# Optimization experiments

Measured on AMD Instinct MI355X. Metric: run time of the kernel, lower is better.

The kernel has to match this reference:

```python
import jax, jax.numpy as jnp
import numpy as np

B, SQ, SK, D, H, F = 8, 512, 1024, 1024, 16, 4096
DK = D // H
NEG_INF = -jnp.inf


def _linear(x, w, b):
    return x @ w + b


def _mha(q, k, v, wq, bq, wk, bk, wv, bv, wo, bo, causal, kv_mask):
    # q: [B,Sq,D], k/v: [B,Sk,D]
    b, sq, d = q.shape
    sk = k.shape[1]
    Q = _linear(q, wq, bq).reshape(b, sq, H, DK).transpose(0, 2, 1, 3)  # [B,H,Sq,dk]
    K = _linear(k, wk, bk).reshape(b, sk, H, DK).transpose(0, 2, 1, 3)
    V = _linear(v, wv, bv).reshape(b, sk, H, DK).transpose(0, 2, 1, 3)
    S = jnp.einsum('bhqd,bhkd->bhqk', Q, K) / jnp.sqrt(jnp.asarray(DK, Q.dtype))
    if kv_mask is not None:
        S = jnp.where(kv_mask[:, None, None, :] == 0, NEG_INF, S)
    if causal:
        tri = jnp.tril(jnp.ones((sq, sk), dtype=bool))
        S = jnp.where(tri, S, NEG_INF)
    A = jax.nn.softmax(S, axis=-1)  # dropout p=0 -> identity
    x = jnp.einsum('bhqk,bhkd->bhqd', A, V).transpose(0, 2, 1, 3).reshape(b, sq, d)
    return _linear(x, wo, bo), A


def _ln(x, g, beta, eps=1e-5):
    mu = jnp.mean(x, axis=-1, keepdims=True)
    var = jnp.mean(jnp.square(x - mu), axis=-1, keepdims=True)
    return (x - mu) * jax.lax.rsqrt(var + eps) * g + beta


def setup_inputs() -> dict:
    key = jax.random.key(0)
    ks = jax.random.split(key, 32)
    s = 0.02
    inp = {
        'x': jax.random.normal(ks[0], (B, SQ, D), jnp.float32),
        'enc_o': jax.random.normal(ks[1], (B, SK, D), jnp.float32),
        'enc_mask': jax.random.randint(ks[2], (B, SK), 0, 2, jnp.int32),
    }
    i = 3
    for pfx in ('a1', 'a2'):
        for nm in ('wq', 'wk', 'wv', 'wo'):
            inp[f'{pfx}_{nm}'] = jax.random.normal(ks[i], (D, D), jnp.float32) * s; i += 1
            inp[f'{pfx}_{nm[1:] and "b" + nm[1:]}'] = jnp.zeros((D,), jnp.float32)
    inp['ff_w1'] = jax.random.normal(ks[i], (D, F), jnp.float32) * s; i += 1
    inp['ff_b1'] = jnp.zeros((F,), jnp.float32)
    inp['ff_w2'] = jax.random.normal(ks[i], (F, D), jnp.float32) * s; i += 1
    inp['ff_b2'] = jnp.zeros((D,), jnp.float32)
    for n in ('ln1', 'ln2', 'ln3'):
        inp[f'{n}_g'] = jnp.ones((D,), jnp.float32)
        inp[f'{n}_b'] = jnp.zeros((D,), jnp.float32)
    return inp


def reference(x, enc_o, enc_mask,
              a1_wq, a1_bq, a1_wk, a1_bk, a1_wv, a1_bv, a1_wo, a1_bo,
              a2_wq, a2_bq, a2_wk, a2_bk, a2_wv, a2_bv, a2_wo, a2_bo,
              ff_w1, ff_b1, ff_w2, ff_b2,
              ln1_g, ln1_b, ln2_g, ln2_b, ln3_g, ln3_b):
    res, _ = _mha(x, x, x, a1_wq, a1_bq, a1_wk, a1_bk, a1_wv, a1_bv, a1_wo, a1_bo,
                  causal=True, kv_mask=None)
    x = _ln(x + res, ln1_g, ln1_b)
    res, attn = _mha(x, enc_o, enc_o, a2_wq, a2_bq, a2_wk, a2_bk, a2_wv, a2_bv, a2_wo, a2_bo,
                     causal=False, kv_mask=enc_mask)
    x = _ln(x + res, ln2_g, ln2_b)
    res = _linear(jax.nn.relu(_linear(x, ff_w1, ff_b1)), ff_w2, ff_b2)
    x = _ln(x + res, ln3_g, ln3_b)
    return (x, attn)
```

## Files before the change

kernel.cpp:

```cpp
#include <hip/hip_runtime.h>
#include <hip/hip_bf16.h>


using bf16 = __hip_bfloat16;
typedef __attribute__((ext_vector_type(8))) short short8;
typedef __attribute__((ext_vector_type(4))) float f32x4;

#define DEVINL __device__ __forceinline__

DEVINL unsigned short bf16bits(float f) {
  __hip_bfloat16 h = __float2bfloat16(f);
  return *reinterpret_cast<unsigned short*>(&h);
}
DEVINL float bits2f(unsigned short u) {
  return __uint_as_float(((unsigned int)u) << 16);
}
DEVINL float tofloat(float f) { return f; }
DEVINL float tofloat(bf16 h) { return __bfloat162float(h); }

#define GLD16(gp, lp) __builtin_amdgcn_global_load_lds( \
    (__attribute__((address_space(1))) const void*)(gp), \
    (__attribute__((address_space(3))) void*)(lp), 16, 0, 0)

struct GemmP {
  const void* A; const bf16* Bt; void* C;
  const float* bias; const int* kmask;
  float scale;
  int M, N, K, lda, ldb, ldc;
  long sAb, sAh, sBb, sBh, sCb, sCh;
};

enum { EPI_BIAS_BF16 = 0, EPI_CAUSAL_BF16, EPI_KMASK_F32, EPI_NONE_BF16,
       EPI_BIAS_F32, EPI_BIAS_RELU_BF16 };

template<int EPI, bool AF32>
__global__ __launch_bounds__(256)
void gemm_k(GemmP p) {
  __shared__ bf16 As[128 * 32];
  __shared__ bf16 Bs[128 * 32];
  const int t = threadIdx.x;
  const int lane = t & 63;
  const int w = t >> 6;
  const int z = blockIdx.z;
  const int zb = z >> 4, zh = z & 15;
  const int m0 = blockIdx.y * 128, n0 = blockIdx.x * 128;

  const bf16* Bb = p.Bt + (long)zb * p.sBb + (long)zh * p.sBh;
  const int fl = lane & 15, fq = lane >> 4;
  const int wm = (w >> 1) * 64, wn = (w & 1) * 64;

  f32x4 acc[4][4];
#pragma unroll
  for (int i = 0; i < 4; ++i)
#pragma unroll
    for (int j = 0; j < 4; ++j) acc[i][j] = (f32x4){0.f, 0.f, 0.f, 0.f};

  const int sr = t >> 2;
  const int sc = (t & 3) * 8;
  char* ldsA = (char*)As + w * 1024;
  char* ldsB = (char*)Bs + w * 1024;

  int brow0 = n0 + sr;      if (brow0 > p.N - 1) brow0 = p.N - 1;
  int brow1 = n0 + sr + 64; if (brow1 > p.N - 1) brow1 = p.N - 1;

  const bf16* Ab16 = nullptr; const float* Af32 = nullptr;
  if (AF32) Af32 = (const float*)p.A + (long)zb * p.sAb + (long)zh * p.sAh;
  else      Ab16 = (const bf16*)p.A + (long)zb * p.sAb + (long)zh * p.sAh;

  for (int k0 = 0; k0 < p.K; k0 += 32) {
    if (!AF32) {
      GLD16(Ab16 + (long)(m0 + sr) * p.lda + k0 + sc, ldsA);
      GLD16(Ab16 + (long)(m0 + sr + 64) * p.lda + k0 + sc, ldsA + 4096);
    } else {
      const int ar = t >> 1, ac = (t & 1) * 16;
      const float* src = Af32 + (long)(m0 + ar) * p.lda + k0 + ac;
      float4 f0 = *(const float4*)(src);
      float4 f1 = *(const float4*)(src + 4);
      float4 f2 = *(const float4*)(src + 8);
      float4 f3 = *(const float4*)(src + 12);
      uint4 q0, q1;
      q0.x = bf16bits(f0.x) | ((unsigned)bf16bits(f0.y) << 16);
      q0.y = bf16bits(f0.z) | ((unsigned)bf16bits(f0.w) << 16);
      q0.z = bf16bits(f1.x) | ((unsigned)bf16bits(f1.y) << 16);
      q0.w = bf16bits(f1.z) | ((unsigned)bf16bits(f1.w) << 16);
      q1.x = bf16bits(f2.x) | ((unsigned)bf16bits(f2.y) << 16);
      q1.y = bf16bits(f2.z) | ((unsigned)bf16bits(f2.w) << 16);
      q1.z = bf16bits(f3.x) | ((unsigned)bf16bits(f3.y) << 16);
      q1.w = bf16bits(f3.z) | ((unsigned)bf16bits(f3.w) << 16);
      *(uint4*)(As + ar * 32 + ac) = q0;
      *(uint4*)(As + ar * 32 + ac + 8) = q1;
    }
    GLD16(Bb + (long)brow0 * p.ldb + k0 + sc, ldsB);
    GLD16(Bb + (long)brow1 * p.ldb + k0 + sc, ldsB + 4096);
    __syncthreads();

    short8 af[4], bfv[4];
#pragma unroll
    for (int i = 0; i < 4; ++i)
      af[i] = *(const short8*)(As + (wm + i * 16 + fl) * 32 + fq * 8);
#pragma unroll
    for (int j = 0; j < 4; ++j)
      bfv[j] = *(const short8*)(Bs + (wn + j * 16 + fl) * 32 + fq * 8);
#pragma unroll
    for (int i = 0; i < 4; ++i)
#pragma unroll
      for (int j = 0; j < 4; ++j)
        acc[i][j] = __builtin_amdgcn_mfma_f32_16x16x32_bf16(af[i], bfv[j], acc[i][j], 0, 0, 0);
    __syncthreads();
  }

  const float NEGINF = -__builtin_inff();
  const long cbase = (long)zb * p.sCb + (long)zh * p.sCh;
#pragma unroll
  for (int i = 0; i < 4; ++i) {
#pragma unroll
    for (int j = 0; j < 4; ++j) {
#pragma unroll
      for (int r = 0; r < 4; ++r) {
        int row = m0 + wm + i * 16 + fq * 4 + r;
        int col = n0 + wn + j * 16 + fl;
        if (col < p.N) {
          float v = acc[i][j][r];
          if (EPI == EPI_BIAS_BF16 || EPI == EPI_BIAS_F32 || EPI == EPI_BIAS_RELU_BF16)
            v += p.bias[col];
          if (EPI == EPI_BIAS_RELU_BF16) v = v > 0.f ? v : 0.f;
          if (EPI == EPI_CAUSAL_BF16) { v *= p.scale; if (col > row) v = NEGINF; }
          if (EPI == EPI_KMASK_F32)   { v *= p.scale; if (p.kmask[zb * 1024 + col] == 0) v = NEGINF; }
          long off = cbase + (long)row * p.ldc + col;
          if (EPI == EPI_KMASK_F32 || EPI == EPI_BIAS_F32) ((float*)p.C)[off] = v;
          else ((bf16*)p.C)[off] = __float2bfloat16(v);
        }
      }
    }
  }
}

__global__ __launch_bounds__(256) void softmax_self_k(bf16* A) {
  const int lane = threadIdx.x & 63;
  const long row = (long)blockIdx.x * 4 + (threadIdx.x >> 6);
  bf16* p = A + row * 512;
  short8 raw = *(const short8*)(p + lane * 8);
  float v[8];
#pragma unroll
  for (int i = 0; i < 8; ++i) v[i] = bits2f((unsigned short)raw[i]);
  float mx = v[0];
#pragma unroll
  for (int i = 1; i < 8; ++i) mx = fmaxf(mx, v[i]);
  for (int off = 32; off; off >>= 1) mx = fmaxf(mx, __shfl_xor(mx, off, 64));
  float s = 0.f;
#pragma unroll
  for (int i = 0; i < 8; ++i) { v[i] = expf(v[i] - mx); s += v[i]; }
  for (int off = 32; off; off >>= 1) s += __shfl_xor(s, off, 64);
  float inv = 1.f / s;
  short8 o;
#pragma unroll
  for (int i = 0; i < 8; ++i) o[i] = (short)bf16bits(v[i] * inv);
  *(short8*)(p + lane * 8) = o;
}

__global__ __launch_bounds__(256) void softmax_cross_k(float* A) {
  const int lane = threadIdx.x & 63;
  const long row = (long)blockIdx.x * 4 + (threadIdx.x >> 6);
  float* p = A + row * 1024;
  float4 v[4];
#pragma unroll
  for (int c = 0; c < 4; ++c) v[c] = *(const float4*)(p + c * 256 + lane * 4);
  float mx = v[0].x;
#pragma unroll
  for (int c = 0; c < 4; ++c) {
    mx = fmaxf(mx, v[c].x); mx = fmaxf(mx, v[c].y);
    mx = fmaxf(mx, v[c].z); mx = fmaxf(mx, v[c].w);
  }
  for (int off = 32; off; off >>= 1) mx = fmaxf(mx, __shfl_xor(mx, off, 64));
  float s = 0.f;
#pragma unroll
  for (int c = 0; c < 4; ++c) {
    v[c].x = expf(v[c].x - mx); s += v[c].x;
    v[c].y = expf(v[c].y - mx); s += v[c].y;
    v[c].z = expf(v[c].z - mx); s += v[c].z;
    v[c].w = expf(v[c].w - mx); s += v[c].w;
  }
  for (int off = 32; off; off >>= 1) s += __shfl_xor(s, off, 64);
  float inv = 1.f / s;
#pragma unroll
  for (int c = 0; c < 4; ++c) {
    v[c].x *= inv; v[c].y *= inv; v[c].z *= inv; v[c].w *= inv;
    *(float4*)(p + c * 256 + lane * 4) = v[c];
  }
}

__global__ __launch_bounds__(256)
void ln_k(const float* __restrict__ x, const float* __restrict__ r,
          const float* __restrict__ g, const float* __restrict__ bt,
          float* __restrict__ outf, bf16* __restrict__ outb) {
  const int lane = threadIdx.x & 63;
  const long row = (long)blockIdx.x * 4 + (threadIdx.x >> 6);
  const float* px = x + row * 1024;
  const float* pr = r + row * 1024;
  float4 v[4];
  float s = 0.f;
#pragma unroll
  for (int c = 0; c < 4; ++c) {
    float4 a = *(const float4*)(px + c * 256 + lane * 4);
    float4 b = *(const float4*)(pr + c * 256 + lane * 4);
    v[c].x = a.x + b.x; v[c].y = a.y + b.y; v[c].z = a.z + b.z; v[c].w = a.w + b.w;
    s += v[c].x + v[c].y + v[c].z + v[c].w;
  }
  for (int off = 32; off; off >>= 1) s += __shfl_xor(s, off, 64);
  float mu = s * (1.f / 1024.f);
  float q = 0.f;
#pragma unroll
  for (int c = 0; c < 4; ++c) {
    float dx = v[c].x - mu, dy = v[c].y - mu, dz = v[c].z - mu, dw = v[c].w - mu;
    q += dx * dx + dy * dy + dz * dz + dw * dw;
  }
  for (int off = 32; off; off >>= 1) q += __shfl_xor(q, off, 64);
  float rs = rsqrtf(q * (1.f / 1024.f) + 1e-5f);
#pragma unroll
  for (int c = 0; c < 4; ++c) {
    int col = c * 256 + lane * 4;
    float4 gg = *(const float4*)(g + col);
    float4 bb = *(const float4*)(bt + col);
    float4 o;
    o.x = (v[c].x - mu) * rs * gg.x + bb.x;
    o.y = (v[c].y - mu) * rs * gg.y + bb.y;
    o.z = (v[c].z - mu) * rs * gg.z + bb.z;
    o.w = (v[c].w - mu) * rs * gg.w + bb.w;
    *(float4*)(outf + row * 1024 + col) = o;
    if (outb) {
      uint2 pk;
      pk.x = bf16bits(o.x) | ((unsigned)bf16bits(o.y) << 16);
      pk.y = bf16bits(o.z) | ((unsigned)bf16bits(o.w) << 16);
      *(uint2*)(outb + row * 1024 + col) = pk;
    }
  }
}

template<typename TI>
__global__ __launch_bounds__(256)
void transpose_k(const TI* __restrict__ in, bf16* __restrict__ out,
                 int R, int C, int ldi, int ldo,
                 long sInb, long sInh, long sOutb, long sOuth) {
  __shared__ float tile[32][33];
  const int zb = blockIdx.z >> 4, zh = blockIdx.z & 15;
  const TI* pin = in + (long)zb * sInb + (long)zh * sInh;
  bf16* pout = out + (long)zb * sOutb + (long)zh * sOuth;
  const int c0 = blockIdx.x * 32, r0 = blockIdx.y * 32;
  const int tx = threadIdx.x & 31, ty = threadIdx.x >> 5;
#pragma unroll
  for (int i = 0; i < 32; i += 8)
    tile[ty + i][tx] = tofloat(pin[(long)(r0 + ty + i) * ldi + c0 + tx]);
  __syncthreads();
#pragma unroll
  for (int i = 0; i < 32; i += 8)
    pout[(long)(c0 + ty + i) * ldo + r0 + tx] = __float2bfloat16(tile[tx][ty + i]);
}

__global__ __launch_bounds__(256) void cvt_k(const float* __restrict__ in,
                                             bf16* __restrict__ out, long n4) {
  long i = (long)blockIdx.x * 256 + threadIdx.x;
  if (i < n4) {
    float4 v = *(const float4*)(in + i * 4);
    uint2 pk;
    pk.x = bf16bits(v.x) | ((unsigned)bf16bits(v.y) << 16);
    pk.y = bf16bits(v.z) | ((unsigned)bf16bits(v.w) << 16);
    *(uint2*)(out + i * 4) = pk;
  }
}

static inline GemmP mkp(const void* A, const bf16* Bt, void* C,
                        const float* bias, const int* km, float sc,
                        int M, int N, int K, int lda, int ldb, int ldc,
                        long sAb, long sAh, long sBb, long sBh, long sCb, long sCh) {
  GemmP p;
  p.A = A; p.Bt = Bt; p.C = C; p.bias = bias; p.kmask = km; p.scale = sc;
  p.M = M; p.N = N; p.K = K; p.lda = lda; p.ldb = ldb; p.ldc = ldc;
  p.sAb = sAb; p.sAh = sAh; p.sBb = sBb; p.sBh = sBh; p.sCb = sCb; p.sCh = sCh;
  return p;
}

extern "C" void kernel_launch(void* const* d_in, const int* in_sizes, int n_in,
                              void* d_out, int out_size, void* d_ws, size_t ws_size,
                              hipStream_t stream) {
  const float* x        = (const float*)d_in[0];
  const float* enc_o    = (const float*)d_in[1];
  const int*   enc_mask = (const int*)d_in[2];
  const float* a1_wq = (const float*)d_in[3];  const float* a1_bq = (const float*)d_in[4];
  const float* a1_wk = (const float*)d_in[5];  const float* a1_bk = (const float*)d_in[6];
  const float* a1_wv = (const float*)d_in[7];  const float* a1_bv = (const float*)d_in[8];
  const float* a1_wo = (const float*)d_in[9];  const float* a1_bo = (const float*)d_in[10];
  const float* a2_wq = (const float*)d_in[11]; const float* a2_bq = (const float*)d_in[12];
  const float* a2_wk = (const float*)d_in[13]; const float* a2_bk = (const float*)d_in[14];
  const float* a2_wv = (const float*)d_in[15]; const float* a2_bv = (const float*)d_in[16];
  const float* a2_wo = (const float*)d_in[17]; const float* a2_bo = (const float*)d_in[18];
  const float* ff_w1 = (const float*)d_in[19]; const float* ff_b1 = (const float*)d_in[20];
  const float* ff_w2 = (const float*)d_in[21]; const float* ff_b2 = (const float*)d_in[22];
  const float* ln1_g = (const float*)d_in[23]; const float* ln1_b = (const float*)d_in[24];
  const float* ln2_g = (const float*)d_in[25]; const float* ln2_b = (const float*)d_in[26];
  const float* ln3_g = (const float*)d_in[27]; const float* ln3_b = (const float*)d_in[28];

  const size_t MB = 1u << 20;
  char* w = (char*)d_ws;
  bf16*  xb   = (bf16*)(w + 0);
  bf16*  encb = (bf16*)(w + 8 * MB);
  float* x1f  = (float*)(w + 24 * MB);
  float* x2f  = (float*)(w + 40 * MB);
  bf16*  xcb  = (bf16*)(w + 56 * MB);
  bf16*  wT   = (bf16*)(w + 64 * MB);
  bf16*  Qb   = (bf16*)(w + 80 * MB);
  bf16*  Kb   = (bf16*)(w + 88 * MB);
  bf16*  Vb   = (bf16*)(w + 104 * MB);
  bf16*  Vt   = (bf16*)(w + 120 * MB);
  bf16*  Ob   = (bf16*)(w + 136 * MB);
  float* res  = (float*)(w + 144 * MB);
  bf16*  Asf  = (bf16*)(w + 160 * MB);

  float* out_x  = (float*)d_out;
  float* attn   = (float*)d_out + 4194304;

  const dim3 blk(256);

  cvt_k<<<4096, blk, 0, stream>>>(x, xb, 1048576);
  cvt_k<<<8192, blk, 0, stream>>>(enc_o, encb, 2097152);

  {
    dim3 tg(32, 32, 1);
    transpose_k<float><<<tg, blk, 0, stream>>>(a1_wq, wT + 0,       1024, 1024, 1024, 1024, 0, 0, 0, 0);
    transpose_k<float><<<tg, blk, 0, stream>>>(a1_wk, wT + 1048576, 1024, 1024, 1024, 1024, 0, 0, 0, 0);
    transpose_k<float><<<tg, blk, 0, stream>>>(a1_wv, wT + 2097152, 1024, 1024, 1024, 1024, 0, 0, 0, 0);
    transpose_k<float><<<tg, blk, 0, stream>>>(a1_wo, wT + 3145728, 1024, 1024, 1024, 1024, 0, 0, 0, 0);
  }
  dim3 gq(8, 32, 1);
  gemm_k<EPI_BIAS_BF16, false><<<gq, blk, 0, stream>>>(
      mkp(xb, wT + 0,       Qb, a1_bq, nullptr, 0.f, 4096, 1024, 1024, 1024, 1024, 1024, 0,0,0,0,0,0));
  gemm_k<EPI_BIAS_BF16, false><<<gq, blk, 0, stream>>>(
      mkp(xb, wT + 1048576, Kb, a1_bk, nullptr, 0.f, 4096, 1024, 1024, 1024, 1024, 1024, 0,0,0,0,0,0));
  gemm_k<EPI_BIAS_BF16, false><<<gq, blk, 0, stream>>>(
      mkp(xb, wT + 2097152, Vb, a1_bv, nullptr, 0.f, 4096, 1024, 1024, 1024, 1024, 1024, 0,0,0,0,0,0));

  gemm_k<EPI_CAUSAL_BF16, false><<<dim3(4, 4, 128), blk, 0, stream>>>(
      mkp(Qb, Kb, Asf, nullptr, nullptr, 0.125f, 512, 512, 64, 1024, 1024, 512,
          524288, 64, 524288, 64, 4194304, 262144));
  softmax_self_k<<<16384, blk, 0, stream>>>(Asf);

  transpose_k<bf16><<<dim3(2, 16, 128), blk, 0, stream>>>(
      Vb, Vt, 512, 64, 1024, 512, 524288, 64, 524288, 32768);

  gemm_k<EPI_NONE_BF16, false><<<dim3(1, 4, 128), blk, 0, stream>>>(
      mkp(Asf, Vt, Ob, nullptr, nullptr, 0.f, 512, 64, 512, 512, 512, 1024,
          4194304, 262144, 524288, 32768, 524288, 64));

  gemm_k<EPI_BIAS_F32, false><<<gq, blk, 0, stream>>>(
      mkp(Ob, wT + 3145728, res, a1_bo, nullptr, 0.f, 4096, 1024, 1024, 1024, 1024, 1024, 0,0,0,0,0,0));

  ln_k<<<1024, blk, 0, stream>>>(x, res, ln1_g, ln1_b, x1f, xcb);

  {
    dim3 tg(32, 32, 1);
    transpose_k<float><<<tg, blk, 0, stream>>>(a2_wq, wT + 0,       1024, 1024, 1024, 1024, 0, 0, 0, 0);
    transpose_k<float><<<tg, blk, 0, stream>>>(a2_wk, wT + 1048576, 1024, 1024, 1024, 1024, 0, 0, 0, 0);
    transpose_k<float><<<tg, blk, 0, stream>>>(a2_wv, wT + 2097152, 1024, 1024, 1024, 1024, 0, 0, 0, 0);
    transpose_k<float><<<tg, blk, 0, stream>>>(a2_wo, wT + 3145728, 1024, 1024, 1024, 1024, 0, 0, 0, 0);
  }
  gemm_k<EPI_BIAS_BF16, false><<<gq, blk, 0, stream>>>(
      mkp(xcb, wT + 0, Qb, a2_bq, nullptr, 0.f, 4096, 1024, 1024, 1024, 1024, 1024, 0,0,0,0,0,0));
  dim3 ge(8, 64, 1);
  gemm_k<EPI_BIAS_BF16, false><<<ge, blk, 0, stream>>>(
      mkp(encb, wT + 1048576, Kb, a2_bk, nullptr, 0.f, 8192, 1024, 1024, 1024, 1024, 1024, 0,0,0,0,0,0));
  gemm_k<EPI_BIAS_BF16, false><<<ge, blk, 0, stream>>>(
      mkp(encb, wT + 2097152, Vb, a2_bv, nullptr, 0.f, 8192, 1024, 1024, 1024, 1024, 1024, 0,0,0,0,0,0));

  gemm_k<EPI_KMASK_F32, false><<<dim3(8, 4, 128), blk, 0, stream>>>(
      mkp(Qb, Kb, attn, nullptr, enc_mask, 0.125f, 512, 1024, 64, 1024, 1024, 1024,
          524288, 64, 1048576, 64, 8388608, 524288));
  softmax_cross_k<<<16384, blk, 0, stream>>>(attn);

  transpose_k<bf16><<<dim3(2, 32, 128), blk, 0, stream>>>(
      Vb, Vt, 1024, 64, 1024, 1024, 1048576, 64, 1048576, 65536);

  gemm_k<EPI_NONE_BF16, true><<<dim3(1, 4, 128), blk, 0, stream>>>(
      mkp(attn, Vt, Ob, nullptr, nullptr, 0.f, 512, 64, 1024, 1024, 1024, 1024,
          8388608, 524288, 1048576, 65536, 524288, 64));

  gemm_k<EPI_BIAS_F32, false><<<gq, blk, 0, stream>>>(
      mkp(Ob, wT + 3145728, res, a2_bo, nullptr, 0.f, 4096, 1024, 1024, 1024, 1024, 1024, 0,0,0,0,0,0));

  ln_k<<<1024, blk, 0, stream>>>(x1f, res, ln2_g, ln2_b, x2f, xcb);

  transpose_k<float><<<dim3(128, 32, 1), blk, 0, stream>>>(
      ff_w1, wT, 1024, 4096, 4096, 1024, 0, 0, 0, 0);
  transpose_k<float><<<dim3(32, 128, 1), blk, 0, stream>>>(
      ff_w2, wT + 4194304, 4096, 1024, 1024, 4096, 0, 0, 0, 0);

  gemm_k<EPI_BIAS_RELU_BF16, false><<<dim3(32, 32, 1), blk, 0, stream>>>(
      mkp(xcb, wT, Asf, ff_b1, nullptr, 0.f, 4096, 4096, 1024, 1024, 1024, 4096, 0,0,0,0,0,0));
  gemm_k<EPI_BIAS_F32, false><<<gq, blk, 0, stream>>>(
      mkp(Asf, wT + 4194304, res, ff_b2, nullptr, 0.f, 4096, 1024, 4096, 4096, 4096, 1024, 0,0,0,0,0,0));

  ln_k<<<1024, blk, 0, stream>>>(x2f, res, ln3_g, ln3_b, out_x, nullptr);
}
```

Measured before the change: 1.192 ms.

## Fuse QKV projections, split-K FFN down-proj, and write bf16 probs from softmax

Concatenates the self-attention Q/K/V weights into one N=3072 GEMM and the cross-attention K/V weights into one N=2048 GEMM, with matching concatenated biases. This cuts launches and reuses the A tile across more columns. The FFN second GEMM (K=4096) now runs as 4-way split-K into fp32 partials, reduced with bias by a separate kernel, to raise parallelism at the cost of extra memory traffic. The cross softmax also writes a bf16 copy of the probabilities, so the PV GEMM loads bf16 asynchronously instead of converting fp32 inline. All weight transposes are hoisted to the start.

```diff
diff --git a/kernel.cpp b/kernel.cpp
--- a/kernel.cpp
+++ b/kernel.cpp
@@ -23,7 +23,7 @@
     (__attribute__((address_space(3))) void*)(lp), 16, 0, 0)
 
 struct GemmP {
-  const void* A; const bf16* Bt; void* C;
+  const bf16* A; const bf16* Bt; void* C;
   const float* bias; const int* kmask;
   float scale;
   int M, N, K, lda, ldb, ldc;
@@ -31,9 +31,9 @@
 };
 
 enum { EPI_BIAS_BF16 = 0, EPI_CAUSAL_BF16, EPI_KMASK_F32, EPI_NONE_BF16,
-       EPI_BIAS_F32, EPI_BIAS_RELU_BF16 };
-
-template<int EPI, bool AF32>
+       EPI_BIAS_F32, EPI_BIAS_RELU_BF16, EPI_PART_F32 };
+
+template<int EPI>
 __global__ __launch_bounds__(256)
 void gemm_k(GemmP p) {
   __shared__ bf16 As[128 * 32];
@@ -45,6 +45,7 @@
   const int zb = z >> 4, zh = z & 15;
   const int m0 = blockIdx.y * 128, n0 = blockIdx.x * 128;
 
+  const bf16* Ab = p.A + (long)zb * p.sAb + (long)zh * p.sAh;
   const bf16* Bb = p.Bt + (long)zb * p.sBb + (long)zh * p.sBh;
   const int fl = lane & 15, fq = lane >> 4;
   const int wm = (w >> 1) * 64, wn = (w & 1) * 64;
@@ -63,33 +64,9 @@
   int brow0 = n0 + sr;      if (brow0 > p.N - 1) brow0 = p.N - 1;
   int brow1 = n0 + sr + 64; if (brow1 > p.N - 1) brow1 = p.N - 1;
 
-  const bf16* Ab16 = nullptr; const float* Af32 = nullptr;
-  if (AF32) Af32 = (const float*)p.A + (long)zb * p.sAb + (long)zh * p.sAh;
-  else      Ab16 = (const bf16*)p.A + (long)zb * p.sAb + (long)zh * p.sAh;
-
   for (int k0 = 0; k0 < p.K; k0 += 32) {
-    if (!AF32) {
-      GLD16(Ab16 + (long)(m0 + sr) * p.lda + k0 + sc, ldsA);
-      GLD16(Ab16 + (long)(m0 + sr + 64) * p.lda + k0 + sc, ldsA + 4096);
-    } else {
-      const int ar = t >> 1, ac = (t & 1) * 16;
-      const float* src = Af32 + (long)(m0 + ar) * p.lda + k0 + ac;
-      float4 f0 = *(const float4*)(src);
-      float4 f1 = *(const float4*)(src + 4);
-      float4 f2 = *(const float4*)(src + 8);
-      float4 f3 = *(const float4*)(src + 12);
-      uint4 q0, q1;
-      q0.x = bf16bits(f0.x) | ((unsigned)bf16bits(f0.y) << 16);
-      q0.y = bf16bits(f0.z) | ((unsigned)bf16bits(f0.w) << 16);
-      q0.z = bf16bits(f1.x) | ((unsigned)bf16bits(f1.y) << 16);
-      q0.w = bf16bits(f1.z) | ((unsigned)bf16bits(f1.w) << 16);
-      q1.x = bf16bits(f2.x) | ((unsigned)bf16bits(f2.y) << 16);
-      q1.y = bf16bits(f2.z) | ((unsigned)bf16bits(f2.w) << 16);
-      q1.z = bf16bits(f3.x) | ((unsigned)bf16bits(f3.y) << 16);
-      q1.w = bf16bits(f3.z) | ((unsigned)bf16bits(f3.w) << 16);
-      *(uint4*)(As + ar * 32 + ac) = q0;
-      *(uint4*)(As + ar * 32 + ac + 8) = q1;
-    }
+    GLD16(Ab + (long)(m0 + sr) * p.lda + k0 + sc, ldsA);
+    GLD16(Ab + (long)(m0 + sr + 64) * p.lda + k0 + sc, ldsA + 4096);
     GLD16(Bb + (long)brow0 * p.ldb + k0 + sc, ldsB);
     GLD16(Bb + (long)brow1 * p.ldb + k0 + sc, ldsB + 4096);
     __syncthreads();
@@ -127,7 +104,8 @@
           if (EPI == EPI_CAUSAL_BF16) { v *= p.scale; if (col > row) v = NEGINF; }
           if (EPI == EPI_KMASK_F32)   { v *= p.scale; if (p.kmask[zb * 1024 + col] == 0) v = NEGINF; }
           long off = cbase + (long)row * p.ldc + col;
-          if (EPI == EPI_KMASK_F32 || EPI == EPI_BIAS_F32) ((float*)p.C)[off] = v;
+          if (EPI == EPI_KMASK_F32 || EPI == EPI_BIAS_F32 || EPI == EPI_PART_F32)
+            ((float*)p.C)[off] = v;
           else ((bf16*)p.C)[off] = __float2bfloat16(v);
         }
       }
@@ -158,7 +136,7 @@
   *(short8*)(p + lane * 8) = o;
 }
 
-__global__ __launch_bounds__(256) void softmax_cross_k(float* A) {
+__global__ __launch_bounds__(256) void softmax_cross_k(float* A, bf16* Pb) {
   const int lane = threadIdx.x & 63;
   const long row = (long)blockIdx.x * 4 + (threadIdx.x >> 6);
   float* p = A + row * 1024;
@@ -186,6 +164,10 @@
   for (int c = 0; c < 4; ++c) {
     v[c].x *= inv; v[c].y *= inv; v[c].z *= inv; v[c].w *= inv;
     *(float4*)(p + c * 256 + lane * 4) = v[c];
+    uint2 pk;
+    pk.x = bf16bits(v[c].x) | ((unsigned)bf16bits(v[c].y) << 16);
+    pk.y = bf16bits(v[c].z) | ((unsigned)bf16bits(v[c].w) << 16);
+    *(uint2*)(Pb + row * 1024 + c * 256 + lane * 4) = pk;
   }
 }
 
@@ -268,12 +250,38 @@
   }
 }
 
+__global__ __launch_bounds__(256)
+void concatb_k(float* dst, const float* a, const float* b, const float* c,
+               int n, int total) {
+  int i = blockIdx.x * 256 + threadIdx.x;
+  if (i >= total) return;
+  float v = (i < n) ? a[i] : (i < 2 * n ? b[i - n] : c[i - 2 * n]);
+  dst[i] = v;
+}
+
+__global__ __launch_bounds__(256)
+void reduce4_k(const float* __restrict__ part, const float* __restrict__ bias,
+               float* __restrict__ out) {
+  long i = ((long)blockIdx.x * 256 + threadIdx.x) * 4;
+  float4 a = *(const float4*)(part + i);
+  float4 b = *(const float4*)(part + 4194304 + i);
+  float4 c = *(const float4*)(part + 2 * 4194304 + i);
+  float4 d = *(const float4*)(part + 3 * 4194304 + i);
+  float4 bi = *(const float4*)(bias + (int)(i & 1023));
+  float4 o;
+  o.x = a.x + b.x + c.x + d.x + bi.x;
+  o.y = a.y + b.y + c.y + d.y + bi.y;
+  o.z = a.z + b.z + c.z + d.z + bi.z;
+  o.w = a.w + b.w + c.w + d.w + bi.w;
+  *(float4*)(out + i) = o;
+}
+
 static inline GemmP mkp(const void* A, const bf16* Bt, void* C,
                         const float* bias, const int* km, float sc,
                         int M, int N, int K, int lda, int ldb, int ldc,
                         long sAb, long sAh, long sBb, long sBh, long sCb, long sCh) {
   GemmP p;
-  p.A = A; p.Bt = Bt; p.C = C; p.bias = bias; p.kmask = km; p.scale = sc;
+  p.A = (const bf16*)A; p.Bt = Bt; p.C = C; p.bias = bias; p.kmask = km; p.scale = sc;
   p.M = M; p.N = N; p.K = K; p.lda = lda; p.ldb = ldb; p.ldc = ldc;
   p.sAb = sAb; p.sAh = sAh; p.sBb = sBb; p.sBh = sBh; p.sCb = sCb; p.sCh = sCh;
   return p;
@@ -300,6 +308,7 @@
   const float* ln3_g = (const float*)d_in[27]; const float* ln3_b = (const float*)d_in[28];
 
   const size_t MB = 1u << 20;
+  const long M1 = 1048576;
   char* w = (char*)d_ws;
   bf16*  xb   = (bf16*)(w + 0);
   bf16*  encb = (bf16*)(w + 8 * MB);
@@ -307,95 +316,94 @@
   float* x2f  = (float*)(w + 40 * MB);
   bf16*  xcb  = (bf16*)(w + 56 * MB);
   bf16*  wT   = (bf16*)(w + 64 * MB);
-  bf16*  Qb   = (bf16*)(w + 80 * MB);
-  bf16*  Kb   = (bf16*)(w + 88 * MB);
-  bf16*  Vb   = (bf16*)(w + 104 * MB);
-  bf16*  Vt   = (bf16*)(w + 120 * MB);
-  bf16*  Ob   = (bf16*)(w + 136 * MB);
-  float* res  = (float*)(w + 144 * MB);
-  bf16*  Asf  = (bf16*)(w + 160 * MB);
-
-  float* out_x  = (float*)d_out;
-  float* attn   = (float*)d_out + 4194304;
+  float* bqkv = (float*)(w + 96 * MB);
+  float* bkv  = (float*)(w + 96 * MB + 16384);
+  bf16*  QKV  = (bf16*)(w + 104 * MB);
+  bf16*  KVc  = (bf16*)(w + 128 * MB);
+  bf16*  Vt   = (bf16*)(w + 160 * MB);
+  bf16*  Ob   = (bf16*)(w + 176 * MB);
+  float* res  = (float*)(w + 184 * MB);
+  float* part = (float*)(w + 200 * MB);
+  bf16*  Asf  = (bf16*)(w + 264 * MB);
+  bf16*  Pb   = (bf16*)(w + 332 * MB);
+
+  float* out_x = (float*)d_out;
+  float* attn  = (float*)d_out + 4194304;
 
   const dim3 blk(256);
 
   cvt_k<<<4096, blk, 0, stream>>>(x, xb, 1048576);
   cvt_k<<<8192, blk, 0, stream>>>(enc_o, encb, 2097152);
-
   {
     dim3 tg(32, 32, 1);
-    transpose_k<float><<<tg, blk, 0, stream>>>(a1_wq, wT + 0,       1024, 1024, 1024, 1024, 0, 0, 0, 0);
-    transpose_k<float><<<tg, blk, 0, stream>>>(a1_wk, wT + 1048576, 1024, 1024, 1024, 1024, 0, 0, 0, 0);
-    transpose_k<float><<<tg, blk, 0, stream>>>(a1_wv, wT + 2097152, 1024, 1024, 1024, 1024, 0, 0, 0, 0);
-    transpose_k<float><<<tg, blk, 0, stream>>>(a1_wo, wT + 3145728, 1024, 1024, 1024, 1024, 0, 0, 0, 0);
-  }
-  dim3 gq(8, 32, 1);
-  gemm_k<EPI_BIAS_BF16, false><<<gq, blk, 0, stream>>>(
-      mkp(xb, wT + 0,       Qb, a1_bq, nullptr, 0.f, 4096, 1024, 1024, 1024, 1024, 1024, 0,0,0,0,0,0));
-  gemm_k<EPI_BIAS_BF16, false><<<gq, blk, 0, stream>>>(
-      mkp(xb, wT + 1048576, Kb, a1_bk, nullptr, 0.f, 4096, 1024, 1024, 1024, 1024, 1024, 0,0,0,0,0,0));
-  gemm_k<EPI_BIAS_BF16, false><<<gq, blk, 0, stream>>>(
-      mkp(xb, wT + 2097152, Vb, a1_bv, nullptr, 0.f, 4096, 1024, 1024, 1024, 1024, 1024, 0,0,0,0,0,0));
-
-  gemm_k<EPI_CAUSAL_BF16, false><<<dim3(4, 4, 128), blk, 0, stream>>>(
-      mkp(Qb, Kb, Asf, nullptr, nullptr, 0.125f, 512, 512, 64, 1024, 1024, 512,
-          524288, 64, 524288, 64, 4194304, 262144));
+    transpose_k<float><<<tg, blk, 0, stream>>>(a1_wq, wT + 0 * M1, 1024, 1024, 1024, 1024, 0,0,0,0);
+    transpose_k<float><<<tg, blk, 0, stream>>>(a1_wk, wT + 1 * M1, 1024, 1024, 1024, 1024, 0,0,0,0);
+    transpose_k<float><<<tg, blk, 0, stream>>>(a1_wv, wT + 2 * M1, 1024, 1024, 1024, 1024, 0,0,0,0);
+    transpose_k<float><<<tg, blk, 0, stream>>>(a1_wo, wT + 3 * M1, 1024, 1024, 1024, 1024, 0,0,0,0);
+    transpose_k<float><<<tg, blk, 0, stream>>>(a2_wq, wT + 4 * M1, 1024, 1024, 1024, 1024, 0,0,0,0);
+    transpose_k<float><<<tg, blk, 0, stream>>>(a2_wk, wT + 5 * M1, 1024, 1024, 1024, 1024, 0,0,0,0);
+    transpose_k<float><<<tg, blk, 0, stream>>>(a2_wv, wT + 6 * M1, 1024, 1024, 1024, 1024, 0,0,0,0);
+    transpose_k<float><<<tg, blk, 0, stream>>>(a2_wo, wT + 7 * M1, 1024, 1024, 1024, 1024, 0,0,0,0);
+    transpose_k<float><<<dim3(128, 32, 1), blk, 0, stream>>>(ff_w1, wT + 8 * M1, 1024, 4096, 4096, 1024, 0,0,0,0);
+    transpose_k<float><<<dim3(32, 128, 1), blk, 0, stream>>>(ff_w2, wT + 12 * M1, 4096, 1024, 1024, 4096, 0,0,0,0);
+  }
+  concatb_k<<<12, blk, 0, stream>>>(bqkv, a1_bq, a1_bk, a1_bv, 1024, 3072);
+  concatb_k<<<8, blk, 0, stream>>>(bkv, a2_bk, a2_bv, a2_bv, 1024, 2048);
+
+  gemm_k<EPI_BIAS_BF16><<<dim3(24, 32, 1), blk, 0, stream>>>(
+      mkp(xb, wT, QKV, bqkv, nullptr, 0.f, 4096, 3072, 1024, 1024, 1024, 3072, 0,0,0,0,0,0));
+  bf16* Qs = QKV;
+  bf16* Ks = QKV + 1024;
+  bf16* Vs = QKV + 2048;
+
+  gemm_k<EPI_CAUSAL_BF16><<<dim3(4, 4, 128), blk, 0, stream>>>(
+      mkp(Qs, Ks, Asf, nullptr, nullptr, 0.125f, 512, 512, 64, 3072, 3072, 512,
+          1572864, 64, 1572864, 64, 4194304, 262144));
   softmax_self_k<<<16384, blk, 0, stream>>>(Asf);
 
   transpose_k<bf16><<<dim3(2, 16, 128), blk, 0, stream>>>(
-      Vb, Vt, 512, 64, 1024, 512, 524288, 64, 524288, 32768);
-
-  gemm_k<EPI_NONE_BF16, false><<<dim3(1, 4, 128), blk, 0, stream>>>(
+      Vs, Vt, 512, 64, 3072, 512, 1572864, 64, 524288, 32768);
+
+  gemm_k<EPI_NONE_BF16><<<dim3(1, 4, 128), blk, 0, stream>>>(
       mkp(Asf, Vt, Ob, nullptr, nullptr, 0.f, 512, 64, 512, 512, 512, 1024,
           4194304, 262144, 524288, 32768, 524288, 64));
 
-  gemm_k<EPI_BIAS_F32, false><<<gq, blk, 0, stream>>>(
-      mkp(Ob, wT + 3145728, res, a1_bo, nullptr, 0.f, 4096, 1024, 1024, 1024, 1024, 1024, 0,0,0,0,0,0));
+  gemm_k<EPI_BIAS_F32><<<dim3(8, 32, 1), blk, 0, stream>>>(
+      mkp(Ob, wT + 3 * M1, res, a1_bo, nullptr, 0.f, 4096, 1024, 1024, 1024, 1024, 1024, 0,0,0,0,0,0));
 
   ln_k<<<1024, blk, 0, stream>>>(x, res, ln1_g, ln1_b, x1f, xcb);
 
-  {
-    dim3 tg(32, 32, 1);
-    transpose_k<float><<<tg, blk, 0, stream>>>(a2_wq, wT + 0,       1024, 1024, 1024, 1024, 0, 0, 0, 0);
-    transpose_k<float><<<tg, blk, 0, stream>>>(a2_wk, wT + 1048576, 1024, 1024, 1024, 1024, 0, 0, 0, 0);
-    transpose_k<float><<<tg, blk, 0, stream>>>(a2_wv, wT + 2097152, 1024, 1024, 1024, 1024, 0, 0, 0, 0);
-    transpose_k<float><<<tg, blk, 0, stream>>>(a2_wo, wT + 3145728, 1024, 1024, 1024, 1024, 0, 0, 0, 0);
-  }
-  gemm_k<EPI_BIAS_BF16, false><<<gq, blk, 0, stream>>>(
-      mkp(xcb, wT + 0, Qb, a2_bq, nullptr, 0.f, 4096, 1024, 1024, 1024, 1024, 1024, 0,0,0,0,0,0));
-  dim3 ge(8, 64, 1);
-  gemm_k<EPI_BIAS_BF16, false><<<ge, blk, 0, stream>>>(
-      mkp(encb, wT + 1048576, Kb, a2_bk, nullptr, 0.f, 8192, 1024, 1024, 1024, 1024, 1024, 0,0,0,0,0,0));
-  gemm_k<EPI_BIAS_BF16, false><<<ge, blk, 0, stream>>>(
-      mkp(encb, wT + 2097152, Vb, a2_bv, nullptr, 0.f, 8192, 1024, 1024, 1024, 1024, 1024, 0,0,0,0,0,0));
-
-  gemm_k<EPI_KMASK_F32, false><<<dim3(8, 4, 128), blk, 0, stream>>>(
-      mkp(Qb, Kb, attn, nullptr, enc_mask, 0.125f, 512, 1024, 64, 1024, 1024, 1024,
-          524288, 64, 1048576, 64, 8388608, 524288));
-  softmax_cross_k<<<16384, blk, 0, stream>>>(attn);
+  gemm_k<EPI_BIAS_BF16><<<dim3(8, 32, 1), blk, 0, stream>>>(
+      mkp(xcb, wT + 4 * M1, QKV, a2_bq, nullptr, 0.f, 4096, 1024, 1024, 1024, 1024, 1024, 0,0,0,0,0,0));
+  gemm_k<EPI_BIAS_BF16><<<dim3(16, 64, 1), blk, 0, stream>>>(
+      mkp(encb, wT + 5 * M1, KVc, bkv, nullptr, 0.f, 8192, 2048, 1024, 1024, 1024, 2048, 0,0,0,0,0,0));
+  bf16* Qc = QKV;
+  bf16* Kc = KVc;
+  bf16* Vc = KVc + 1024;
+
+  gemm_k<EPI_KMASK_F32><<<dim3(8, 4, 128), blk, 0, stream>>>(
+      mkp(Qc, Kc, attn, nullptr, enc_mask, 0.125f, 512, 1024, 64, 1024, 2048, 1024,
+          524288, 64, 2097152, 64, 8388608, 524288));
+  softmax_cross_k<<<16384, blk, 0, stream>>>(attn, Pb);
 
   transpose_k<bf16><<<dim3(2, 32, 128), blk, 0, stream>>>(
-      Vb, Vt, 1024, 64, 1024, 1024, 1048576, 64, 1048576, 65536);
-
-  gemm_k<EPI_NONE_BF16, true><<<dim3(1, 4, 128), blk, 0, stream>>>(
-      mkp(attn, Vt, Ob, nullptr, nullptr, 0.f, 512, 64, 1024, 1024, 1024, 1024,
+      Vc, Vt, 1024, 64, 2048, 1024, 2097152, 64, 1048576, 65536);
+
+  gemm_k<EPI_NONE_BF16><<<dim3(1, 4, 128), blk, 0, stream>>>(
+      mkp(Pb, Vt, Ob, nullptr, nullptr, 0.f, 512, 64, 1024, 1024, 1024, 1024,
           8388608, 524288, 1048576, 65536, 524288, 64));
 
-  gemm_k<EPI_BIAS_F32, false><<<gq, blk, 0, stream>>>(
-      mkp(Ob, wT + 3145728, res, a2_bo, nullptr, 0.f, 4096, 1024, 1024, 1024, 1024, 1024, 0,0,0,0,0,0));
+  gemm_k<EPI_BIAS_F32><<<dim3(8, 32, 1), blk, 0, stream>>>(
+      mkp(Ob, wT + 7 * M1, res, a2_bo, nullptr, 0.f, 4096, 1024, 1024, 1024, 1024, 1024, 0,0,0,0,0,0));
 
   ln_k<<<1024, blk, 0, stream>>>(x1f, res, ln2_g, ln2_b, x2f, xcb);
 
-  transpose_k<float><<<dim3(128, 32, 1), blk, 0, stream>>>(
-      ff_w1, wT, 1024, 4096, 4096, 1024, 0, 0, 0, 0);
-  transpose_k<float><<<dim3(32, 128, 1), blk, 0, stream>>>(
-      ff_w2, wT + 4194304, 4096, 1024, 1024, 4096, 0, 0, 0, 0);
-
-  gemm_k<EPI_BIAS_RELU_BF16, false><<<dim3(32, 32, 1), blk, 0, stream>>>(
-      mkp(xcb, wT, Asf, ff_b1, nullptr, 0.f, 4096, 4096, 1024, 1024, 1024, 4096, 0,0,0,0,0,0));
-  gemm_k<EPI_BIAS_F32, false><<<gq, blk, 0, stream>>>(
-      mkp(Asf, wT + 4194304, res, ff_b2, nullptr, 0.f, 4096, 1024, 4096, 4096, 4096, 1024, 0,0,0,0,0,0));
+  gemm_k<EPI_BIAS_RELU_BF16><<<dim3(32, 32, 1), blk, 0, stream>>>(
+      mkp(xcb, wT + 8 * M1, Asf, ff_b1, nullptr, 0.f, 4096, 4096, 1024, 1024, 1024, 4096, 0,0,0,0,0,0));
+  gemm_k<EPI_PART_F32><<<dim3(8, 32, 4), blk, 0, stream>>>(
+      mkp(Asf, wT + 12 * M1, part, nullptr, nullptr, 0.f, 4096, 1024, 1024, 4096, 4096, 1024,
+          0, 1024, 0, 1024, 0, 4194304));
+  reduce4_k<<<4096, blk, 0, stream>>>(part, ff_b2, res);
 
   ln_k<<<1024, blk, 0, stream>>>(x2f, res, ln3_g, ln3_b, out_x, nullptr);
 }
```

Measured after the change: 1.155 ms. 1.03x faster.
